# Performance work log

Measured on AMD Instinct MI355X. Metric: run time of the kernel, lower is better.

## Reference

```python
import jax, jax.numpy as jnp
import numpy as np

S = 256
H = 4       # n_heads
DH = 32     # head_dim
D = H * DH  # model dim
EPS = 1e-5


def setup_inputs() -> dict:
    key = jax.random.key(0)
    ks = jax.random.split(key, 12)
    x = jax.random.normal(ks[0], (1, S, S, D), dtype=jnp.float32)
    # attention mask: mostly 0, occasionally large negative (masked)
    keep = jax.random.uniform(ks[1], (1, 1, S, S)) < 0.9
    attn_mask = jnp.where(keep, 0.0, -1e9).astype(jnp.float32)
    sc = 1.0 / np.sqrt(D)
    ln_w = jnp.ones((D,), jnp.float32)
    ln_b = jnp.zeros((D,), jnp.float32)
    Wb = jax.random.normal(ks[2], (H, D), jnp.float32) * sc   # bias projection (linear.weight)
    Wq = jax.random.normal(ks[3], (D, D), jnp.float32) * sc
    Wk = jax.random.normal(ks[4], (D, D), jnp.float32) * sc
    Wv = jax.random.normal(ks[5], (D, D), jnp.float32) * sc
    Wg = jax.random.normal(ks[6], (D, D), jnp.float32) * sc
    Wo = jax.random.normal(ks[7], (D, D), jnp.float32) * sc
    return {"x": x, "attn_mask": attn_mask, "ln_w": ln_w, "ln_b": ln_b,
            "Wb": Wb, "Wq": Wq, "Wk": Wk, "Wv": Wv, "Wg": Wg, "Wo": Wo}


def reference(x, attn_mask, ln_w, ln_b, Wb, Wq, Wk, Wv, Wg, Wo):
    # x: [1,S,S,D] pair representation; ending=False so no transpose of S axes.
    x0 = x[0]  # [S,S,D]
    mu = jnp.mean(x0, axis=-1, keepdims=True)
    var = jnp.mean(jnp.square(x0 - mu), axis=-1, keepdims=True)
    xn = (x0 - mu) * jax.lax.rsqrt(var + EPS) * ln_w + ln_b  # [S,S,D]

    # triangle bias: [S,S,H] -> [1,H,S,S] (broadcast over batch-of-rows)
    bias = jnp.einsum('bqd,hd->hbq', xn, Wb)[None]  # [1,H,S,S]

    def heads(W):
        return jnp.einsum('bqd,ed->bqe', xn, W).reshape(S, S, H, DH).transpose(0, 2, 1, 3)

    q, k, v = heads(Wq), heads(Wk), heads(Wv)  # each [S,H,S,DH]

    scale = 1.0 / np.sqrt(DH)
    scores = jnp.einsum('bhqd,bhkd->bhqk', q, k) * scale + bias + attn_mask  # [S,H,S,S]
    attn = jax.nn.softmax(scores, axis=-1)
    o = jnp.einsum('bhqk,bhkd->bhqd', attn, v)  # [S,H,S,DH]
    o = o.transpose(0, 2, 1, 3).reshape(S, S, D)

    g = jnp.einsum('bqd,ed->bqe', xn, Wg)
    out = jnp.einsum('bqe,fe->bqf', o * jax.nn.sigmoid(g), Wo)  # [S,S,D]
    return out[None]  # [1,S,S,D]
```

## Files before the change

### kernel.cpp

```cpp
#include <hip/hip_runtime.h>
#include <hip/hip_bf16.h>

#define S_DIM 256
#define D_DIM 128
#define H_DIM 4
#define NPOS  (S_DIM * S_DIM)
#define SW    384
#define LOG2E 1.4426950408889634f

typedef __attribute__((ext_vector_type(8))) short  short8;
typedef __attribute__((ext_vector_type(4))) float  f32x4;

__device__ __forceinline__ float b2f(unsigned short u) {
    union { float f; unsigned int u32; } c; c.u32 = ((unsigned int)u) << 16; return c.f;
}
__device__ __forceinline__ unsigned short f2b(float f) {
    __hip_bfloat16 h = __float2bfloat16(f);
    return *reinterpret_cast<unsigned short*>(&h);
}

__global__ __launch_bounds__(256) void wconv_kernel(
    const float* __restrict__ Wq, const float* __restrict__ Wk,
    const float* __restrict__ Wv, const float* __restrict__ Wg,
    const float* __restrict__ Wo, unsigned short* __restrict__ wbf)
{
    const int gy = blockIdx.y;
    const float* W = (gy == 0) ? Wq : (gy == 1) ? Wk : (gy == 2) ? Wv
                   : (gy == 3) ? Wg : Wo;
    const int idx = (blockIdx.x * 256 + threadIdx.x) * 8;
    float4 f0 = *(const float4*)(W + idx);
    float4 f1 = *(const float4*)(W + idx + 4);
    unsigned short pk[8] = {f2b(f0.x), f2b(f0.y), f2b(f0.z), f2b(f0.w),
                            f2b(f1.x), f2b(f1.y), f2b(f1.z), f2b(f1.w)};
    *(uint4*)(wbf + (size_t)gy * 16384 + idx) = *(const uint4*)pk;
}

__global__ __launch_bounds__(256) void ln_biasmask_kernel(
    const float* __restrict__ x, const float* __restrict__ mask,
    const float* __restrict__ lnw, const float* __restrict__ lnb,
    const float* __restrict__ Wb, float* __restrict__ bm)
{
    const int wave = threadIdx.x >> 6, lane = threadIdx.x & 63;
    const int p = blockIdx.x * 4 + wave;

    float2 v = ((const float2*)x)[p * 64 + lane];
    float s = v.x + v.y, ss = v.x * v.x + v.y * v.y;
    #pragma unroll
    for (int m = 1; m < 64; m <<= 1) { s += __shfl_xor(s, m); ss += __shfl_xor(ss, m); }
    float mean = s * (1.f / 128.f);
    float var  = ss * (1.f / 128.f) - mean * mean;
    float rstd = rsqrtf(var + 1e-5f);

    float xn0 = (v.x - mean) * rstd * lnw[lane * 2]     + lnb[lane * 2];
    float xn1 = (v.y - mean) * rstd * lnw[lane * 2 + 1] + lnb[lane * 2 + 1];

    float mval = mask[p];
    #pragma unroll
    for (int h = 0; h < H_DIM; h++) {
        float d = xn0 * Wb[h * 128 + lane * 2] + xn1 * Wb[h * 128 + lane * 2 + 1];
        #pragma unroll
        for (int m = 1; m < 64; m <<= 1) d += __shfl_xor(d, m);
        if (lane == 0) bm[(long)h * NPOS + p] = (d + mval) * LOG2E;
    }
}

template<int FUSE_BIAS>
__global__ __launch_bounds__(512) void proj_ln_kernel(
    const float* __restrict__ x, const float* __restrict__ mask,
    const float* __restrict__ lnw, const float* __restrict__ lnb,
    const float* __restrict__ Wb, const unsigned short* __restrict__ wbf,
    int p0, unsigned short* __restrict__ strip, unsigned short* __restrict__ vt,
    float* __restrict__ bm)
{
    __shared__ __align__(16) unsigned short A_lds[128 * 136];
    __shared__ __align__(16) unsigned short W_lds[128 * 136];
    const int tid = threadIdx.x;
    const int m0 = blockIdx.x * 128;
    const int lr = tid >> 4, c8 = (tid & 15) * 8;

    float4 wb0[4], wb1[4];
    if (FUSE_BIAS) {
        #pragma unroll
        for (int hh = 0; hh < 4; hh++) {
            wb0[hh] = *(const float4*)(Wb + hh * 128 + c8);
            wb1[hh] = *(const float4*)(Wb + hh * 128 + c8 + 4);
        }
    }

    #pragma unroll
    for (int i = 0; i < 4; i++) {
        int row = lr + i * 32;
        int p   = p0 + m0 + row;
        const float* src = x + (size_t)p * 128 + c8;
        float4 f0 = *(const float4*)(src);
        float4 f1 = *(const float4*)(src + 4);
        float s  = f0.x + f0.y + f0.z + f0.w + f1.x + f1.y + f1.z + f1.w;
        float ss = f0.x*f0.x + f0.y*f0.y + f0.z*f0.z + f0.w*f0.w
                 + f1.x*f1.x + f1.y*f1.y + f1.z*f1.z + f1.w*f1.w;
        #pragma unroll
        for (int m = 1; m < 16; m <<= 1) { s += __shfl_xor(s, m); ss += __shfl_xor(ss, m); }
        float mean = s * (1.f / 128.f);
        float var  = ss * (1.f / 128.f) - mean * mean;
        float rstd = rsqrtf(var + 1e-5f);
        float xv[8] = {f0.x, f0.y, f0.z, f0.w, f1.x, f1.y, f1.z, f1.w};
        float xl[8];
        unsigned short pk[8];
        #pragma unroll
        for (int j = 0; j < 8; j++) {
            xl[j] = (xv[j] - mean) * rstd * lnw[c8 + j] + lnb[c8 + j];
            pk[j] = f2b(xl[j]);
        }
        *(uint4*)(&A_lds[row * 136 + c8]) = *(const uint4*)pk;

        if (FUSE_BIAS) {
            float mv = 0.f;
            if ((tid & 15) == 0) mv = mask[p];
            #pragma unroll
            for (int hh = 0; hh < 4; hh++) {
                float bh = xl[0]*wb0[hh].x + xl[1]*wb0[hh].y
                         + xl[2]*wb0[hh].z + xl[3]*wb0[hh].w
                         + xl[4]*wb1[hh].x + xl[5]*wb1[hh].y
                         + xl[6]*wb1[hh].z + xl[7]*wb1[hh].w;
                #pragma unroll
                for (int mk = 1; mk < 16; mk <<= 1) bh += __shfl_xor(bh, mk);
                if ((tid & 15) == 0) bm[(long)hh * NPOS + p] = (bh + mv) * LOG2E;
            }
        }
    }
    __syncthreads();

    const int w = tid >> 6, lane = tid & 63;
    const int l16 = lane & 15, quad = lane >> 4;

    short8 a4[4];
    #pragma unroll
    for (int k0i = 0; k0i < 4; k0i++)
        a4[k0i] = *(const short8*)(&A_lds[(w * 16 + l16) * 136 + k0i * 32 + quad * 8]);

    #pragma unroll 1
    for (int gy = 0; gy < 4; gy++) {
        if (gy > 0) __syncthreads();
        const uint4* wsrc = (const uint4*)(wbf + (size_t)gy * 16384);
        #pragma unroll
        for (int j = 0; j < 4; j++) {
            int idx = tid + j * 512;
            int row = idx >> 4, cc = (idx & 15) * 8;
            *(uint4*)(&W_lds[row * 136 + cc]) = wsrc[idx];
        }
        __syncthreads();

        f32x4 acc[8];
        #pragma unroll
        for (int nt = 0; nt < 8; nt++) acc[nt] = (f32x4){0.f, 0.f, 0.f, 0.f};

        if (gy == 2) {
            #pragma unroll
            for (int k0i = 0; k0i < 4; k0i++)
                #pragma unroll
                for (int nt = 0; nt < 8; nt++) {
                    short8 b = *(const short8*)(&W_lds[(nt * 16 + l16) * 136 + k0i * 32 + quad * 8]);
                    acc[nt] = __builtin_amdgcn_mfma_f32_16x16x32_bf16(a4[k0i], b, acc[nt], 0, 0, 0);
                }
            const int blv = m0 >> 8;
            const int kl  = (m0 & 255) + w * 16 + quad * 4;
            #pragma unroll
            for (int nt = 0; nt < 8; nt++) {
                uint2 pk;
                pk.x = (unsigned)f2b(acc[nt][0]) | ((unsigned)f2b(acc[nt][1]) << 16);
                pk.y = (unsigned)f2b(acc[nt][2]) | ((unsigned)f2b(acc[nt][3]) << 16);
                *(uint2*)(&vt[((size_t)(blv * 128 + nt * 16 + l16)) * 256 + kl]) = pk;
            }
        } else {
            #pragma unroll
            for (int k0i = 0; k0i < 4; k0i++)
                #pragma unroll
                for (int nt = 0; nt < 8; nt++) {
                    short8 b = *(const short8*)(&W_lds[(nt * 16 + l16) * 136 + k0i * 32 + quad * 8]);
                    acc[nt] = __builtin_amdgcn_mfma_f32_16x16x32_bf16(b, a4[k0i], acc[nt], 0, 0, 0);
                }
            const int off = (gy == 0) ? 0 : (gy == 1) ? 128 : 256;
            const size_t rowbase = (size_t)(m0 + w * 16 + l16) * SW + off;
            #pragma unroll
            for (int nt = 0; nt < 8; nt++) {
                uint2 pk;
                pk.x = (unsigned)f2b(acc[nt][0]) | ((unsigned)f2b(acc[nt][1]) << 16);
                pk.y = (unsigned)f2b(acc[nt][2]) | ((unsigned)f2b(acc[nt][3]) << 16);
                *(uint2*)(&strip[rowbase + nt * 16 + quad * 4]) = pk;
            }
        }
    }
}

__global__ __launch_bounds__(512) void attn_kernel(
    const unsigned short* __restrict__ strip, const unsigned short* __restrict__ vt,
    const float* __restrict__ bm, int b0, unsigned short* __restrict__ gated)
{
    const int bl = blockIdx.x;
    const int b  = b0 + bl;
    const int tid = threadIdx.x;
    const int w = tid >> 6, lane = tid & 63;
    const int h  = (blockIdx.y << 1) + (w >> 2);
    const int wq = w & 3;
    const int l16 = lane & 15, quad = lane >> 4;
    const float* bmh = bm + (long)h * NPOS;
    const unsigned short* vth = vt + ((size_t)bl * 128 + h * 32) * 256;
    const float scale2 = 0.17677669529663687f * LOG2E;

    #pragma unroll 1
    for (int i = 0; i < 4; i++) {
        const int q0 = (wq * 4 + i) * 16;
        short8 bq = *(const short8*)(strip + (size_t)(bl * 256 + q0 + l16) * SW + h * 32 + quad * 8);
        const float* brow = bmh + (size_t)(q0 + l16) * 256 + quad * 4;

        float sc[16][4];
        #pragma unroll
        for (int nt = 0; nt < 16; nt++) {
            short8 ka = *(const short8*)(strip + (size_t)(bl * 256 + nt * 16 + l16) * SW + 128 + h * 32 + quad * 8);
            f32x4 c = (f32x4){0.f, 0.f, 0.f, 0.f};
            c = __builtin_amdgcn_mfma_f32_16x16x32_bf16(ka, bq, c, 0, 0, 0);
            float4 bb = *(const float4*)(brow + nt * 16);
            sc[nt][0] = c[0] * scale2 + bb.x;
            sc[nt][1] = c[1] * scale2 + bb.y;
            sc[nt][2] = c[2] * scale2 + bb.z;
            sc[nt][3] = c[3] * scale2 + bb.w;
        }

        float s0 = 0.f, s1 = 0.f, s2 = 0.f, s3 = 0.f;
        f32x4 oaccA[2], oaccB[2];
        oaccA[0] = (f32x4){0.f, 0.f, 0.f, 0.f};
        oaccA[1] = (f32x4){0.f, 0.f, 0.f, 0.f};
        oaccB[0] = (f32x4){0.f, 0.f, 0.f, 0.f};
        oaccB[1] = (f32x4){0.f, 0.f, 0.f, 0.f};
        #pragma unroll
        for (int kt = 0; kt < 8; kt++) {
            const int na = kt * 2, nb = kt * 2 + 1;
            float e0 = exp2f(sc[na][0]); s0 += e0;
            float e1 = exp2f(sc[na][1]); s1 += e1;
            float e2 = exp2f(sc[na][2]); s2 += e2;
            float e3 = exp2f(sc[na][3]); s3 += e3;
            float f0_ = exp2f(sc[nb][0]); s0 += f0_;
            float f1_ = exp2f(sc[nb][1]); s1 += f1_;
            float f2_ = exp2f(sc[nb][2]); s2 += f2_;
            float f3_ = exp2f(sc[nb][3]); s3 += f3_;
            union { unsigned int u[4]; short8 s; } pu;
            pu.u[0] = (unsigned)f2b(e0)  | ((unsigned)f2b(e1)  << 16);
            pu.u[1] = (unsigned)f2b(e2)  | ((unsigned)f2b(e3)  << 16);
            pu.u[2] = (unsigned)f2b(f0_) | ((unsigned)f2b(f1_) << 16);
            pu.u[3] = (unsigned)f2b(f2_) | ((unsigned)f2b(f3_) << 16);
            short8 pa = pu.s;
            f32x4* dst = (kt & 1) ? oaccB : oaccA;
            #pragma unroll
            for (int nh = 0; nh < 2; nh++) {
                const unsigned short* vrow = vth + (size_t)(nh * 16 + l16) * 256 + kt * 32 + quad * 4;
                uint2 vlo = *(const uint2*)(vrow);
                uint2 vhi = *(const uint2*)(vrow + 16);
                union { unsigned int u[4]; short8 s; } vu;
                vu.u[0] = vlo.x; vu.u[1] = vlo.y;
                vu.u[2] = vhi.x; vu.u[3] = vhi.y;
                dst[nh] = __builtin_amdgcn_mfma_f32_16x16x32_bf16(pa, vu.s, dst[nh], 0, 0, 0);
            }
        }
        float ssum = (s0 + s1) + (s2 + s3);
        ssum += __shfl_xor(ssum, 16);
        ssum += __shfl_xor(ssum, 32);
        float inv = 1.f / ssum;

        #pragma unroll
        for (int rr = 0; rr < 4; rr++) {
            float invr = __shfl(inv, quad * 4 + rr);
            int row = q0 + quad * 4 + rr;
            #pragma unroll
            for (int nh = 0; nh < 2; nh++) {
                int cl = nh * 16 + l16;
                float g = b2f(strip[(size_t)(bl * 256 + row) * SW + 256 + h * 32 + cl]);
                float ov = (oaccA[nh][rr] + oaccB[nh][rr]) * invr;
                ov = ov / (1.f + __expf(-g));
                gated[((size_t)b * 256 + row) * 128 + h * 32 + cl] = f2b(ov);
            }
        }
    }
}

__global__ __launch_bounds__(256) void outproj_mfma_kernel(
    const unsigned short* __restrict__ gated, const unsigned short* __restrict__ wbf,
    float* __restrict__ out)
{
    __shared__ __align__(16) unsigned short Wo_lds[128 * 136];
    const int tid = threadIdx.x, m0 = blockIdx.x * 64;
    const int w = tid >> 6, lane = tid & 63;
    const int l16 = lane & 15, quad = lane >> 4;

    {
        const uint4* wsrc = (const uint4*)(wbf + (size_t)4 * 16384);
        #pragma unroll
        for (int j = 0; j < 8; j++) {
            int idx = tid + j * 256;
            int row = idx >> 4, cc = (idx & 15) * 8;
            *(uint4*)(&Wo_lds[row * 136 + cc]) = wsrc[idx];
        }
    }

    const unsigned short* arow = gated + (size_t)(m0 + w * 16 + l16) * 128;
    short8 a4[4];
    #pragma unroll
    for (int k0i = 0; k0i < 4; k0i++)
        a4[k0i] = *(const short8*)(arow + k0i * 32 + quad * 8);
    __syncthreads();

    f32x4 acc[8];
    #pragma unroll
    for (int nt = 0; nt < 8; nt++) acc[nt] = (f32x4){0.f, 0.f, 0.f, 0.f};

    #pragma unroll
    for (int k0i = 0; k0i < 4; k0i++)
        #pragma unroll
        for (int nt = 0; nt < 8; nt++) {
            short8 b = *(const short8*)(&Wo_lds[(nt * 16 + l16) * 136 + k0i * 32 + quad * 8]);
            acc[nt] = __builtin_amdgcn_mfma_f32_16x16x32_bf16(b, a4[k0i], acc[nt], 0, 0, 0);
        }

    float* orow = out + (size_t)(m0 + w * 16 + l16) * 128;
    #pragma unroll
    for (int nt = 0; nt < 8; nt++)
        *(f32x4*)(&orow[nt * 16 + quad * 4]) = acc[nt];
}

extern "C" void kernel_launch(void* const* d_in, const int* in_sizes, int n_in,
                              void* d_out, int out_size, void* d_ws, size_t ws_size,
                              hipStream_t stream)
{
    (void)in_sizes; (void)n_in; (void)out_size;
    const float* x    = (const float*)d_in[0];
    const float* mask = (const float*)d_in[1];
    const float* lnw  = (const float*)d_in[2];
    const float* lnb  = (const float*)d_in[3];
    const float* Wb   = (const float*)d_in[4];
    const float* Wq   = (const float*)d_in[5];
    const float* Wk   = (const float*)d_in[6];
    const float* Wv   = (const float*)d_in[7];
    const float* Wg   = (const float*)d_in[8];
    const float* Wo   = (const float*)d_in[9];
    float* out = (float*)d_out;

    const size_t bmB = (size_t)H_DIM * NPOS * sizeof(float);
    const size_t gB  = (size_t)NPOS * 128 * sizeof(unsigned short);
    const size_t wB  = (size_t)5 * 16384 * sizeof(unsigned short);
    const size_t perRow = (size_t)256 * SW * 2 + (size_t)128 * 256 * 2;
    int HB = 256;
    while (HB > 16 && bmB + gB + wB + (size_t)HB * perRow > ws_size) HB >>= 1;

    char* ws = (char*)d_ws;
    float*          bm    = (float*)ws;
    unsigned short* gated = (unsigned short*)(ws + bmB);
    unsigned short* wbf   = (unsigned short*)(ws + bmB + gB);
    unsigned short* vt    = (unsigned short*)(ws + bmB + gB + wB);
    unsigned short* strip = vt + (size_t)HB * 128 * 256;

    wconv_kernel<<<dim3(8, 5), 256, 0, stream>>>(Wq, Wk, Wv, Wg, Wo, wbf);

    if (HB == 256) {
        proj_ln_kernel<1><<<dim3(512), 512, 0, stream>>>(
            x, mask, lnw, lnb, Wb, wbf, 0, strip, vt, bm);
        attn_kernel<<<dim3(256, 2), 512, 0, stream>>>(strip, vt, bm, 0, gated);
    } else {
        ln_biasmask_kernel<<<NPOS / 4, 256, 0, stream>>>(x, mask, lnw, lnb, Wb, bm);
        for (int b0 = 0; b0 < S_DIM; b0 += HB) {
            proj_ln_kernel<0><<<dim3(HB * 2), 512, 0, stream>>>(
                x, mask, lnw, lnb, Wb, wbf, b0 * 256, strip, vt, bm);
            attn_kernel<<<dim3(HB, 2), 512, 0, stream>>>(strip, vt, bm, b0, gated);
        }
    }
    outproj_mfma_kernel<<<NPOS / 64, 256, 0, stream>>>(gated, wbf, out);
}
```

Baseline: 204.1 us.

## Fuse QK score computation into PV loop to drop score register array

Removes the separate pass that computed all 16 score tiles into a 64-float register array before the softmax/PV loop. Instead, each PV iteration computes its two QK MFMA tiles, adds bias, and exponentiates immediately. The loop is also partially unrolled by 2 instead of fully. This is meant to cut register pressure and possibly raise occupancy for the 512-thread blocks, at the cost of less independent work for latency hiding of the global K and bias loads.

```diff
diff --git a/kernel.cpp b/kernel.cpp
--- a/kernel.cpp
+++ b/kernel.cpp
@@ -204,6 +204,7 @@
     const int l16 = lane & 15, quad = lane >> 4;
     const float* bmh = bm + (long)h * NPOS;
     const unsigned short* vth = vt + ((size_t)bl * 128 + h * 32) * 256;
+    const unsigned short* kbase = strip + (size_t)(bl * 256 + l16) * SW + 128 + h * 32 + quad * 8;
     const float scale2 = 0.17677669529663687f * LOG2E;
 
     #pragma unroll 1
@@ -211,19 +212,6 @@
         const int q0 = (wq * 4 + i) * 16;
         short8 bq = *(const short8*)(strip + (size_t)(bl * 256 + q0 + l16) * SW + h * 32 + quad * 8);
         const float* brow = bmh + (size_t)(q0 + l16) * 256 + quad * 4;
-
-        float sc[16][4];
-        #pragma unroll
-        for (int nt = 0; nt < 16; nt++) {
-            short8 ka = *(const short8*)(strip + (size_t)(bl * 256 + nt * 16 + l16) * SW + 128 + h * 32 + quad * 8);
-            f32x4 c = (f32x4){0.f, 0.f, 0.f, 0.f};
-            c = __builtin_amdgcn_mfma_f32_16x16x32_bf16(ka, bq, c, 0, 0, 0);
-            float4 bb = *(const float4*)(brow + nt * 16);
-            sc[nt][0] = c[0] * scale2 + bb.x;
-            sc[nt][1] = c[1] * scale2 + bb.y;
-            sc[nt][2] = c[2] * scale2 + bb.z;
-            sc[nt][3] = c[3] * scale2 + bb.w;
-        }
 
         float s0 = 0.f, s1 = 0.f, s2 = 0.f, s3 = 0.f;
         f32x4 oaccA[2], oaccB[2];
@@ -231,17 +219,25 @@
         oaccA[1] = (f32x4){0.f, 0.f, 0.f, 0.f};
         oaccB[0] = (f32x4){0.f, 0.f, 0.f, 0.f};
         oaccB[1] = (f32x4){0.f, 0.f, 0.f, 0.f};
-        #pragma unroll
+        #pragma unroll 2
         for (int kt = 0; kt < 8; kt++) {
             const int na = kt * 2, nb = kt * 2 + 1;
-            float e0 = exp2f(sc[na][0]); s0 += e0;
-            float e1 = exp2f(sc[na][1]); s1 += e1;
-            float e2 = exp2f(sc[na][2]); s2 += e2;
-            float e3 = exp2f(sc[na][3]); s3 += e3;
-            float f0_ = exp2f(sc[nb][0]); s0 += f0_;
-            float f1_ = exp2f(sc[nb][1]); s1 += f1_;
-            float f2_ = exp2f(sc[nb][2]); s2 += f2_;
-            float f3_ = exp2f(sc[nb][3]); s3 += f3_;
+            short8 ka0 = *(const short8*)(kbase + (size_t)(na * 16) * SW);
+            short8 ka1 = *(const short8*)(kbase + (size_t)(nb * 16) * SW);
+            f32x4 c0 = (f32x4){0.f, 0.f, 0.f, 0.f};
+            f32x4 c1 = (f32x4){0.f, 0.f, 0.f, 0.f};
+            c0 = __builtin_amdgcn_mfma_f32_16x16x32_bf16(ka0, bq, c0, 0, 0, 0);
+            c1 = __builtin_amdgcn_mfma_f32_16x16x32_bf16(ka1, bq, c1, 0, 0, 0);
+            float4 bb0 = *(const float4*)(brow + na * 16);
+            float4 bb1 = *(const float4*)(brow + nb * 16);
+            float e0 = exp2f(c0[0] * scale2 + bb0.x); s0 += e0;
+            float e1 = exp2f(c0[1] * scale2 + bb0.y); s1 += e1;
+            float e2 = exp2f(c0[2] * scale2 + bb0.z); s2 += e2;
+            float e3 = exp2f(c0[3] * scale2 + bb0.w); s3 += e3;
+            float f0_ = exp2f(c1[0] * scale2 + bb1.x); s0 += f0_;
+            float f1_ = exp2f(c1[1] * scale2 + bb1.y); s1 += f1_;
+            float f2_ = exp2f(c1[2] * scale2 + bb1.z); s2 += f2_;
+            float f3_ = exp2f(c1[3] * scale2 + bb1.w); s3 += f3_;
             union { unsigned int u[4]; short8 s; } pu;
             pu.u[0] = (unsigned)f2b(e0)  | ((unsigned)f2b(e1)  << 16);
             pu.u[1] = (unsigned)f2b(e2)  | ((unsigned)f2b(e3)  << 16);
```

Result: slower. 255.4 us (+25.1%).
